# Optimization experiments

Measured on AMD Instinct MI355X. Metric: run time of the kernel, lower is better.

Reference implementation:

```python
import jax, jax.numpy as jnp
import numpy as np
import math

B, N, D = 4, 1024, 1024
H = 16
HD = D // H          # 64
TOP_K = 64
NUM_STATIC = 32


def setup_inputs() -> dict:
    key = jax.random.key(0)
    ks = jax.random.split(key, 10)
    s = 1.0 / math.sqrt(D)  # ~ nn.Linear default init scale
    inp = {
        "x": jax.random.normal(ks[0], (B, N, D), dtype=jnp.float32),
        "Wq": jax.random.uniform(ks[1], (D, D), jnp.float32, -s, s),
        "bq": jax.random.uniform(ks[2], (D,), jnp.float32, -s, s),
        "Wk": jax.random.uniform(ks[3], (D, D), jnp.float32, -s, s),
        "bk": jax.random.uniform(ks[4], (D,), jnp.float32, -s, s),
        "Wv": jax.random.uniform(ks[5], (D, D), jnp.float32, -s, s),
        "bv": jax.random.uniform(ks[6], (D,), jnp.float32, -s, s),
        "Wo": jax.random.uniform(ks[7], (D, D), jnp.float32, -s, s),
        "bo": jax.random.uniform(ks[8], (D,), jnp.float32, -s, s),
        "static_keys": jax.random.normal(ks[9], (NUM_STATIC, D), dtype=jnp.float32),
    }
    return inp


def _heads(t):
    # [B, N, D] -> [B, H, N, HD]
    return t.reshape(B, N, H, HD).transpose(0, 2, 1, 3)


def reference(x, Wq, bq, Wk, bk, Wv, bv, Wo, bo, static_keys):
    Q = _heads(x @ Wq.T + bq)
    K = _heads(x @ Wk.T + bk)
    V = _heads(x @ Wv.T + bv)

    # Replace the first NUM_STATIC key slots with learned static keys.
    K_stat = static_keys.reshape(1, NUM_STATIC, H, HD).transpose(0, 2, 1, 3)  # [1,H,S,HD]
    K_stat = jnp.broadcast_to(K_stat, (B, H, NUM_STATIC, HD))
    K = jnp.concatenate([K_stat, K[:, :, NUM_STATIC:, :]], axis=2)  # [B,H,N,HD]

    scores = jnp.einsum("bhnd,bhmd->bhnm", Q, K) / math.sqrt(HD)  # [B,H,N,N]

    # top-k mask: keep top_k scores per query, -inf elsewhere
    top_scores, top_idx = jax.lax.top_k(scores, TOP_K)  # [B,H,N,K]
    bi = jnp.arange(B)[:, None, None, None]
    hi = jnp.arange(H)[None, :, None, None]
    ni = jnp.arange(N)[None, None, :, None]
    masked = jnp.full(scores.shape, -jnp.inf, dtype=scores.dtype)
    masked = masked.at[bi, hi, ni, top_idx].set(top_scores)

    attn = jax.nn.softmax(masked, axis=-1)
    out = jnp.einsum("bhnm,bhmd->bhnd", attn, V)  # [B,H,N,HD]
    out = out.transpose(0, 2, 1, 3).reshape(B, N, D)
    return out @ Wo.T + bo
```

## Files before the change

### kernel.cpp

```cpp
#include <hip/hip_runtime.h>

#define NSTAT 32
#define MAXSEL 76

typedef __attribute__((ext_vector_type(8))) short bf16x8_t;
typedef __attribute__((ext_vector_type(4))) float f32x4_t;

#define GLOAD_LDS16(g, l) \
    __builtin_amdgcn_global_load_lds((const __attribute__((address_space(1))) void*)(g), \
                                     (__attribute__((address_space(3))) void*)(l), 16, 0, 0)

__device__ __forceinline__ ushort rtn_bf16(float a) {
    unsigned u = __float_as_uint(a);
    return (ushort)((u + 0x7FFFu + ((u >> 16) & 1u)) >> 16);
}
__device__ __forceinline__ void limb2(float a, ushort& h, ushort& l) {
    ushort hh = rtn_bf16(a);
    float fh = __uint_as_float(((unsigned)hh) << 16);
    float r1 = a - fh;
    l = rtn_bf16(r1);
    h = hh;
}

__global__ __launch_bounds__(256)
void decomp_w_kernel(const float* __restrict__ Wq, const float* __restrict__ Wk,
                     const float* __restrict__ Wv, const float* __restrict__ Wo,
                     ushort* __restrict__ WLq, ushort* __restrict__ WoLb)
{
    const int m = blockIdx.y;
    const float* src = (m == 0) ? Wq : (m == 1) ? Wk : (m == 2) ? Wv : Wo;
    const int idx = blockIdx.x * 256 + threadIdx.x;
    const int e8 = idx * 8;
    const int row = e8 >> 10, k0 = e8 & 1023;
    const int kt = k0 >> 5, q = (k0 >> 3) & 3;
    const size_t doff = ((size_t)row << 10) + (size_t)(kt * 32) + (size_t)((q ^ (row & 3)) * 8);

    float4 v0 = *(const float4*)(src + e8);
    float4 v1 = *(const float4*)(src + e8 + 4);
    float f[8] = {v0.x, v0.y, v0.z, v0.w, v1.x, v1.y, v1.z, v1.w};

    const size_t Mi = (size_t)1 << 20;
    ushort h[8], l[8];
    #pragma unroll
    for (int e = 0; e < 8; ++e) limb2(f[e], h[e], l[e]);
    ushort* H = (m == 3) ? WoLb : WLq + (size_t)(m * 2) * Mi;
    ushort* L = H + Mi;
    *(ushort4*)(H + doff)     = make_ushort4(h[0],h[1],h[2],h[3]);
    *(ushort4*)(H + doff + 4) = make_ushort4(h[4],h[5],h[6],h[7]);
    *(ushort4*)(L + doff)     = make_ushort4(l[0],l[1],l[2],l[3]);
    *(ushort4*)(L + doff + 4) = make_ushort4(l[4],l[5],l[6],l[7]);
}

__global__ __launch_bounds__(256, 3)
void limb_gemm_kernel(const float* __restrict__ A,
                      const ushort* __restrict__ WLq, const ushort* __restrict__ WoLb,
                      const float* __restrict__ bq, const float* __restrict__ bk,
                      const float* __restrict__ bv, const float* __restrict__ bo,
                      const float* __restrict__ statk,
                      float* __restrict__ Qw, float* __restrict__ Vw,
                      ushort* __restrict__ KHo, ushort* __restrict__ KLo,
                      float* __restrict__ Cout, int is_out)
{
    __shared__ __align__(16) ushort Al[2][128][32];
    __shared__ __align__(16) ushort Bl[2][2][128][32];

    const int t = threadIdx.x;
    const int bx = blockIdx.x, by = blockIdx.y;
    const int mode = is_out ? 3 : (int)blockIdx.z;
    const int wc0 = bx * 128;
    const int arow0 = by * 128;

    const size_t Mi = (size_t)1 << 20;
    const ushort* BpH;
    const float* bias;
    if (mode == 0)      { BpH = WLq;          bias = bq; }
    else if (mode == 1) { BpH = WLq + 2*Mi;   bias = bk; }
    else if (mode == 2) { BpH = WLq + 4*Mi;   bias = bv; }
    else                { BpH = WoLb;         bias = bo; }
    const ushort* BpL = BpH + Mi;

    const int ll = t & 63, w = t >> 6;

    f32x4_t acc[4][4];
    #pragma unroll
    for (int i = 0; i < 4; ++i)
        #pragma unroll
        for (int j = 0; j < 4; ++j) acc[i][j] = (f32x4_t){0.f, 0.f, 0.f, 0.f};

    auto stageB = [&](int kt, int bb) {
        #pragma unroll
        for (int limb = 0; limb < 2; ++limb) {
            const ushort* src = limb ? BpL : BpH;
            #pragma unroll
            for (int call = 0; call < 2; ++call) {
                int chunk = (w * 2 + call) * 64 + ll;
                int eoff = chunk * 8;
                int row = eoff >> 5, qp = (eoff >> 3) & 3;
                const ushort* g = src + ((size_t)(wc0 + row) << 10) + kt * 32 + qp * 8;
                char* l = ((char*)&Bl[bb][limb][0][0]) + (w * 2 + call) * 1024;
                GLOAD_LDS16(g, l);
            }
        }
    };
    const int srow = t >> 1, skh = (t & 1) * 16;
    auto loadA = [&](int kt, float4* a4) {
        const float* p = A + (((size_t)(arow0 + srow)) << 10) + kt * 32 + skh;
        a4[0] = *(const float4*)(p + 0);
        a4[1] = *(const float4*)(p + 4);
        a4[2] = *(const float4*)(p + 8);
        a4[3] = *(const float4*)(p + 12);
    };
    auto writeA = [&](const float4* a4) {
        float f[16];
        #pragma unroll
        for (int i = 0; i < 4; ++i) {
            f[i*4+0] = a4[i].x; f[i*4+1] = a4[i].y; f[i*4+2] = a4[i].z; f[i*4+3] = a4[i].w;
        }
        ushort h[16], lo[16];
        #pragma unroll
        for (int e = 0; e < 16; ++e) limb2(f[e], h[e], lo[e]);
        const int sw = srow & 3;
        #pragma unroll
        for (int qq = 0; qq < 2; ++qq) {
            int q = (skh >> 3) + qq;
            int qo = (q ^ sw) * 8;
            bf16x8_t vH, vL;
            #pragma unroll
            for (int e = 0; e < 8; ++e) {
                vH[e] = (short)h[qq*8+e]; vL[e] = (short)lo[qq*8+e];
            }
            *(bf16x8_t*)&Al[0][srow][qo] = vH;
            *(bf16x8_t*)&Al[1][srow][qo] = vL;
        }
    };

    const int wr = (w >> 1) * 64, wcv = (w & 1) * 64;
    const int fr = ll & 15, kg = ll >> 4;

    auto compute = [&](int bb) {
        bf16x8_t af[4][2];
        #pragma unroll
        for (int i = 0; i < 4; ++i) {
            int row = wr + i * 16 + fr;
            int qo = (kg ^ (row & 3)) * 8;
            af[i][0] = *(const bf16x8_t*)&Al[0][row][qo];
            af[i][1] = *(const bf16x8_t*)&Al[1][row][qo];
        }
        #pragma unroll
        for (int j = 0; j < 4; ++j) {
            int row = wcv + j * 16 + fr;
            int qo = (kg ^ (row & 3)) * 8;
            bf16x8_t b0 = *(const bf16x8_t*)&Bl[bb][0][row][qo];
            bf16x8_t b1 = *(const bf16x8_t*)&Bl[bb][1][row][qo];
            #pragma unroll
            for (int i = 0; i < 4; ++i) {
                acc[i][j] = __builtin_amdgcn_mfma_f32_16x16x32_bf16(af[i][0], b0, acc[i][j], 0, 0, 0);
                acc[i][j] = __builtin_amdgcn_mfma_f32_16x16x32_bf16(af[i][0], b1, acc[i][j], 0, 0, 0);
                acc[i][j] = __builtin_amdgcn_mfma_f32_16x16x32_bf16(af[i][1], b0, acc[i][j], 0, 0, 0);
            }
        }
    };

    float4 a4[4];
    loadA(0, a4);
    writeA(a4);
    stageB(0, 0);
    __syncthreads();

    float4 a4n[4];
    for (int kt = 0; kt < 32; ++kt) {
        int bb = kt & 1;
        if (kt < 31) {
            stageB(kt + 1, bb ^ 1);
            loadA(kt + 1, a4n);
        }
        compute(bb);
        __syncthreads();
        if (kt < 31) writeA(a4n);
        __syncthreads();
    }

    #pragma unroll
    for (int i = 0; i < 4; ++i) {
        #pragma unroll
        for (int j = 0; j < 4; ++j) {
            int c = wc0 + wcv + j * 16 + (ll & 15);
            float bv_ = bias[c];
            #pragma unroll
            for (int q = 0; q < 4; ++q) {
                int gr = arow0 + wr + i * 16 + (kg) * 4 + q;
                float v = acc[i][j][q] + bv_;
                if (mode == 3) {
                    Cout[(size_t)gr * 1024 + c] = v;
                } else {
                    int b = gr >> 10, n = gr & 1023;
                    int h = c >> 6, d = c & 63;
                    size_t bhn = ((size_t)(b * 16 + h)) * 1024 + n;
                    if (mode == 1) {
                        if (n < NSTAT) v = statk[n * 1024 + c];
                        ushort kh, klo;
                        limb2(v, kh, klo);
                        size_t off = bhn * 64 + (size_t)(((d >> 3) ^ (n & 7)) * 8) + (d & 7);
                        KHo[off] = kh;
                        KLo[off] = klo;
                    } else {
                        float* Out = (mode == 0) ? Qw : Vw;
                        Out[bhn * 64 + d] = v;
                    }
                }
            }
        }
    }
}

__device__ __forceinline__ void radix_stage7(int* __restrict__ hist, int r, int l,
                                             const unsigned* __restrict__ ku,
                                             unsigned pref, unsigned mask, int shift,
                                             int tgt, int2* __restrict__ piv)
{
    #pragma unroll
    for (int b = 0; b < 8; ++b) hist[(l*8 + b)*33 + r] = 0;
    __syncthreads();
    #pragma unroll
    for (int j = 0; j < 64; ++j) {
        unsigned k = ku[j];
        if ((k & mask) == pref)
            atomicAdd(&hist[(int)((k >> shift) & 127u)*33 + r], 1);
    }
    __syncthreads();
    int seg = 0;
    #pragma unroll
    for (int b = 0; b < 8; ++b) seg += hist[(l*8 + b)*33 + r];
    int suf = seg;
    #pragma unroll
    for (int off = 1; off < 16; off <<= 1) {
        int v = __shfl_down(suf, off, 16);
        suf += (l + off < 16) ? v : 0;
    }
    const int above = suf - seg;
    if (above < tgt && above + seg >= tgt) {
        int c = above;
        #pragma unroll
        for (int b = 7; b >= 0; --b) {
            int h = hist[(l*8 + b)*33 + r];
            if (c + h >= tgt) { piv[r] = make_int2(l*8 + b, tgt - c); break; }
            c += h;
        }
    }
    __syncthreads();
}

__global__ __launch_bounds__(512, 4)
void attn_mfma_kernel(const float* __restrict__ Qw,
                      const ushort* __restrict__ KH, const ushort* __restrict__ KL,
                      const float* __restrict__ Vw, float* __restrict__ outp)
{
    __shared__ __align__(16) char pool[59904];
    __shared__ int2 piv[32];
    __shared__ int cnt[32];
    __shared__ float rowsum[32];

    int* hist = (int*)pool;
    float (*Qs)[68] = (float(*)[68])(pool + 32768);
    uint2 (*sel)[MAXSEL] = (uint2(*)[MAXSEL])pool;

    const int t = threadIdx.x;
    const int bid0 = blockIdx.x;
    const int bid = (bid0 & 7) * 256 + (bid0 >> 3);
    const int qt = bid & 31;
    const int bh = bid >> 5;
    const int n0 = qt * 32;
    const float* Qbase = Qw + ((size_t)bh * 1024 + n0) * 64;
    const float* Vbase = Vw + (size_t)bh * 1024 * 64;
    const ushort* KHb = KH + (size_t)bh * 1024 * 64;
    const ushort* KLb = KL + (size_t)bh * 1024 * 64;

    const int ll = t & 63;
    const int w  = t >> 6;
    const int qh = w >> 2;
    const int kr = w & 3;
    const int r  = t >> 4, l = t & 15;

    {
        int q = t >> 4, dq = (t & 15) * 4;
        *(float4*)&Qs[q][dq] = *(const float4*)(Qbase + q * 64 + dq);
    }
    auto stageK = [&](int c, int kb) {
        const ushort* gH = KHb + (size_t)c * 4096 + t * 8;
        const ushort* gL = KLb + (size_t)c * 4096 + t * 8;
        char* dH = pool + kb * 16384 + t * 16;
        char* dL = pool + kb * 16384 + 8192 + t * 16;
        GLOAD_LDS16(gH, dH);
        GLOAD_LDS16(gL, dL);
    };
    stageK(0, 0);
    if (t < 32) cnt[t] = 0;
    __syncthreads();

    bf16x8_t aH[2], aL[2];
    {
        const int arow = qh * 16 + (ll & 15), akg = ll >> 4;
        #pragma unroll
        for (int s = 0; s < 2; ++s) {
            const float* qp = &Qs[arow][s*32 + akg*8];
            float4 q0 = *(const float4*)qp;
            float4 q1 = *(const float4*)(qp + 4);
            float qv[8] = {q0.x,q0.y,q0.z,q0.w,q1.x,q1.y,q1.z,q1.w};
            #pragma unroll
            for (int j = 0; j < 8; ++j) {
                ushort hh, lo2;
                limb2(qv[j], hh, lo2);
                aH[s][j] = (short)hh; aL[s][j] = (short)lo2;
            }
        }
    }

    unsigned ku[64];

    #pragma unroll
    for (int c = 0; c < 16; ++c) {
        const int kb = c & 1;
        float (*scb)[72] = (float(*)[72])(pool + 41472 + kb * 9216);
        if (c < 15) stageK(c + 1, kb ^ 1);

        {
            const ushort* KH_l = (const ushort*)(pool + kb * 16384);
            const ushort* KL_l = KH_l + 4096;
            const int brow = kr * 16 + (ll & 15);
            f32x4_t a_ = {0.f, 0.f, 0.f, 0.f};
            #pragma unroll
            for (int s = 0; s < 2; ++s) {
                int q2 = (s*4 + (ll >> 4)) ^ (brow & 7);
                int off = brow*64 + q2*8;
                bf16x8_t bH = *(const bf16x8_t*)&KH_l[off];
                bf16x8_t bL = *(const bf16x8_t*)&KL_l[off];
                a_ = __builtin_amdgcn_mfma_f32_16x16x32_bf16(aH[s], bH, a_, 0, 0, 0);
                a_ = __builtin_amdgcn_mfma_f32_16x16x32_bf16(aH[s], bL, a_, 0, 0, 0);
                a_ = __builtin_amdgcn_mfma_f32_16x16x32_bf16(aL[s], bH, a_, 0, 0, 0);
            }
            const int qr = qh * 16 + (ll >> 4) * 4;
            scb[qr+0][brow] = a_[0];
            scb[qr+1][brow] = a_[1];
            scb[qr+2][brow] = a_[2];
            scb[qr+3][brow] = a_[3];
        }
        __syncthreads();

        {
            float4 v4 = *(const float4*)&scb[r][l*4];
            float vv[4] = {v4.x, v4.y, v4.z, v4.w};
            #pragma unroll
            for (int e = 0; e < 4; ++e) {
                float vc = fminf(fmaxf(vv[e], -31.9f), 31.9f);
                ku[c*4 + e] = (unsigned)(int)fmaf(vc, 32768.f, 1048576.f);
            }
        }
    }

    int tgt = 64;
    radix_stage7(hist, r, l, ku, 0u, 0u, 14, tgt, piv);
    unsigned pref = (unsigned)piv[r].x << 14; tgt = piv[r].y;
    radix_stage7(hist, r, l, ku, pref, 0x1FC000u, 7, tgt, piv);
    pref |= (unsigned)piv[r].x << 7; tgt = piv[r].y;
    radix_stage7(hist, r, l, ku, pref, 0x1FFF80u, 0, tgt, piv);
    const unsigned thr = pref | (unsigned)piv[r].x;

    const unsigned bhi = thr + 2u;
    const unsigned blo = thr - 2u;
    #pragma unroll
    for (int j = 0; j < 64; ++j) {
        unsigned k = ku[j];
        if (k >= blo) {
            int slot = atomicAdd(&cnt[r], 1);
            if (slot < MAXSEL)
                sel[r][slot] = make_uint2((unsigned)((j >> 2)*64 + l*4 + (j & 3)), k);
        }
    }
    __syncthreads();

    {
        int cc = cnt[r]; cc = (cc < MAXSEL) ? cc : MAXSEL;
        int Dl = 0, ml = 0;
        for (int j = l; j < cc; j += 16) {
            unsigned k = sel[r][j].y;
            if (k > bhi) Dl++; else ml++;
        }
        #pragma unroll
        for (int off = 8; off; off >>= 1) {
            Dl += __shfl_xor(Dl, off, 16);
            ml += __shfl_xor(ml, off, 16);
        }
        const float frac = (float)(64 - Dl) / (float)ml;
        float ls = 0.f;
        for (int j = l; j < cc; j += 16) {
            uint2 p = sel[r][j];
            float wgt = __expf((float)(int)(p.y - thr) * 3.814697265625e-6f);
            if (p.y <= bhi) wgt *= frac;
            p.y = __float_as_uint(wgt);
            sel[r][j] = p;
            ls += wgt;
        }
        #pragma unroll
        for (int off = 8; off; off >>= 1) ls += __shfl_xor(ls, off, 16);
        if (l == 0) { rowsum[r] = ls; cnt[r] = cc; }
    }
    __syncthreads();

    {
        const int pr = t >> 4;
        const int d4 = (t & 15) * 4;
        const int bb = bh >> 4, hh = bh & 15;
        const int cc = cnt[pr];
        float4 a = make_float4(0.f, 0.f, 0.f, 0.f);
        int j = 0;
        for (; j + 1 < cc; j += 2) {
            uint2 p0 = sel[pr][j];
            uint2 p1 = sel[pr][j+1];
            float w0 = __uint_as_float(p0.y);
            float w1 = __uint_as_float(p1.y);
            float4 v0 = *(const float4*)(Vbase + (size_t)p0.x * 64 + d4);
            float4 v1 = *(const float4*)(Vbase + (size_t)p1.x * 64 + d4);
            a.x += w0 * v0.x + w1 * v1.x;
            a.y += w0 * v0.y + w1 * v1.y;
            a.z += w0 * v0.z + w1 * v1.z;
            a.w += w0 * v0.w + w1 * v1.w;
        }
        if (j < cc) {
            uint2 p = sel[pr][j];
            float wv = __uint_as_float(p.y);
            float4 v = *(const float4*)(Vbase + (size_t)p.x * 64 + d4);
            a.x += wv * v.x; a.y += wv * v.y; a.z += wv * v.z; a.w += wv * v.w;
        }
        float inv = 1.0f / rowsum[pr];
        a.x *= inv; a.y *= inv; a.z *= inv; a.w *= inv;
        *(float4*)(outp + ((size_t)bb * 1024 + (n0 + pr)) * 1024 + hh * 64 + d4) = a;
    }
}

extern "C" void kernel_launch(void* const* d_in, const int* in_sizes, int n_in,
                              void* d_out, int out_size, void* d_ws, size_t ws_size,
                              hipStream_t stream) {
    const float* x     = (const float*)d_in[0];
    const float* Wq    = (const float*)d_in[1];
    const float* bq    = (const float*)d_in[2];
    const float* Wk    = (const float*)d_in[3];
    const float* bk    = (const float*)d_in[4];
    const float* Wv    = (const float*)d_in[5];
    const float* bv    = (const float*)d_in[6];
    const float* Wo    = (const float*)d_in[7];
    const float* bo    = (const float*)d_in[8];
    const float* statk = (const float*)d_in[9];
    float* out = (float*)d_out;
    char* base = (char*)d_ws;

    const size_t MiB = (size_t)1 << 20;
    float*  Qw   = (float*)(base);
    float*  Vw   = (float*)(base + 16*MiB);
    ushort* KH   = (ushort*)(base + 32*MiB);
    ushort* KL   = (ushort*)(base + 40*MiB);
    ushort* WoLb = (ushort*)(base + 48*MiB);
    ushort* WLq  = (ushort*)(base + 52*MiB);
    float*  op   = (float*)(base + 52*MiB);

    dim3 gd(512, 4);
    decomp_w_kernel<<<gd, 256, 0, stream>>>(Wq, Wk, Wv, Wo, WLq, WoLb);

    dim3 g1(8, 32, 3);
    limb_gemm_kernel<<<g1, 256, 0, stream>>>(x, WLq, WoLb, bq, bk, bv, bo, statk,
                                             Qw, Vw, KH, KL, nullptr, 0);

    attn_mfma_kernel<<<2048, 512, 0, stream>>>(Qw, KH, KL, Vw, op);

    dim3 g2(8, 32, 1);
    limb_gemm_kernel<<<g2, 256, 0, stream>>>(op, WLq, WoLb, bq, bk, bv, bo, statk,
                                             Qw, Vw, KH, KL, out, 1);
}
```

Before: 320.4 us.

## Keep QK scores in MFMA register layout, process 128-key chunks, drop score LDS buffer

The score loop now handles 128 keys per iteration with two accumulators per wave and packs the MFMA outputs straight into each thread's radix keys. This removes the LDS score transpose buffer and one barrier-mediated round trip per chunk. The radix histograms now index rows by the MFMA layout and keep per-row prefixes for the four rows each thread owns. K staging is single-buffered, with the next chunk loaded after a sync, which shrinks LDS so occupancy can rise (launch bounds 4 to 6 waves) but loses the prefetch overlap with compute.

```diff
diff --git a/kernel.cpp b/kernel.cpp
--- a/kernel.cpp
+++ b/kernel.cpp
@@ -213,53 +213,18 @@
     }
 }
 
-__device__ __forceinline__ void radix_stage7(int* __restrict__ hist, int r, int l,
-                                             const unsigned* __restrict__ ku,
-                                             unsigned pref, unsigned mask, int shift,
-                                             int tgt, int2* __restrict__ piv)
-{
-    #pragma unroll
-    for (int b = 0; b < 8; ++b) hist[(l*8 + b)*33 + r] = 0;
-    __syncthreads();
-    #pragma unroll
-    for (int j = 0; j < 64; ++j) {
-        unsigned k = ku[j];
-        if ((k & mask) == pref)
-            atomicAdd(&hist[(int)((k >> shift) & 127u)*33 + r], 1);
-    }
-    __syncthreads();
-    int seg = 0;
-    #pragma unroll
-    for (int b = 0; b < 8; ++b) seg += hist[(l*8 + b)*33 + r];
-    int suf = seg;
-    #pragma unroll
-    for (int off = 1; off < 16; off <<= 1) {
-        int v = __shfl_down(suf, off, 16);
-        suf += (l + off < 16) ? v : 0;
-    }
-    const int above = suf - seg;
-    if (above < tgt && above + seg >= tgt) {
-        int c = above;
-        #pragma unroll
-        for (int b = 7; b >= 0; --b) {
-            int h = hist[(l*8 + b)*33 + r];
-            if (c + h >= tgt) { piv[r] = make_int2(l*8 + b, tgt - c); break; }
-            c += h;
-        }
-    }
-    __syncthreads();
-}
-
-__global__ __launch_bounds__(512, 4)
+__global__ __launch_bounds__(512, 6)
 void attn_mfma_kernel(const float* __restrict__ Qw,
                       const ushort* __restrict__ KH, const ushort* __restrict__ KL,
                       const float* __restrict__ Vw, float* __restrict__ outp)
 {
-    __shared__ __align__(16) char pool[59904];
+    __shared__ __align__(16) char pool[41472];
     __shared__ int2 piv[32];
     __shared__ int cnt[32];
     __shared__ float rowsum[32];
 
+    ushort* Klds0 = (ushort*)pool;
+    ushort* Klds1 = Klds0 + 8192;
     int* hist = (int*)pool;
     float (*Qs)[68] = (float(*)[68])(pool + 32768);
     uint2 (*sel)[MAXSEL] = (uint2(*)[MAXSEL])pool;
@@ -280,20 +245,22 @@
     const int qh = w >> 2;
     const int kr = w & 3;
     const int r  = t >> 4, l = t & 15;
+    const int qr = qh * 16 + (ll >> 4) * 4;
 
     {
         int q = t >> 4, dq = (t & 15) * 4;
         *(float4*)&Qs[q][dq] = *(const float4*)(Qbase + q * 64 + dq);
     }
-    auto stageK = [&](int c, int kb) {
-        const ushort* gH = KHb + (size_t)c * 4096 + t * 8;
-        const ushort* gL = KLb + (size_t)c * 4096 + t * 8;
-        char* dH = pool + kb * 16384 + t * 16;
-        char* dL = pool + kb * 16384 + 8192 + t * 16;
-        GLOAD_LDS16(gH, dH);
-        GLOAD_LDS16(gL, dL);
-    };
-    stageK(0, 0);
+    auto stageK = [&](int c) {
+        const size_t cb = (size_t)c * 8192;
+        #pragma unroll
+        for (int i = 0; i < 2; ++i) {
+            int boff = i * 8192 + w * 1024;
+            GLOAD_LDS16(KHb + cb + boff / 2 + ll * 8, ((char*)Klds0) + boff);
+            GLOAD_LDS16(KLb + cb + boff / 2 + ll * 8, ((char*)Klds1) + boff);
+        }
+    };
+    stageK(0);
     if (t < 32) cnt[t] = 0;
     __syncthreads();
 
@@ -318,72 +285,107 @@
     unsigned ku[64];
 
     #pragma unroll
-    for (int c = 0; c < 16; ++c) {
-        const int kb = c & 1;
-        float (*scb)[72] = (float(*)[72])(pool + 41472 + kb * 9216);
-        if (c < 15) stageK(c + 1, kb ^ 1);
-
+    for (int c = 0; c < 8; ++c) {
+        f32x4_t acc0 = {0.f,0.f,0.f,0.f}, acc1 = {0.f,0.f,0.f,0.f};
         {
-            const ushort* KH_l = (const ushort*)(pool + kb * 16384);
-            const ushort* KL_l = KH_l + 4096;
-            const int brow = kr * 16 + (ll & 15);
-            f32x4_t a_ = {0.f, 0.f, 0.f, 0.f};
+            const int brow0 = kr * 32 + (ll & 15);
+            const int brow1 = brow0 + 16;
             #pragma unroll
             for (int s = 0; s < 2; ++s) {
-                int q2 = (s*4 + (ll >> 4)) ^ (brow & 7);
-                int off = brow*64 + q2*8;
-                bf16x8_t bH = *(const bf16x8_t*)&KH_l[off];
-                bf16x8_t bL = *(const bf16x8_t*)&KL_l[off];
-                a_ = __builtin_amdgcn_mfma_f32_16x16x32_bf16(aH[s], bH, a_, 0, 0, 0);
-                a_ = __builtin_amdgcn_mfma_f32_16x16x32_bf16(aH[s], bL, a_, 0, 0, 0);
-                a_ = __builtin_amdgcn_mfma_f32_16x16x32_bf16(aL[s], bH, a_, 0, 0, 0);
-            }
-            const int qr = qh * 16 + (ll >> 4) * 4;
-            scb[qr+0][brow] = a_[0];
-            scb[qr+1][brow] = a_[1];
-            scb[qr+2][brow] = a_[2];
-            scb[qr+3][brow] = a_[3];
-        }
-        __syncthreads();
-
-        {
-            float4 v4 = *(const float4*)&scb[r][l*4];
-            float vv[4] = {v4.x, v4.y, v4.z, v4.w};
-            #pragma unroll
-            for (int e = 0; e < 4; ++e) {
-                float vc = fminf(fmaxf(vv[e], -31.9f), 31.9f);
-                ku[c*4 + e] = (unsigned)(int)fmaf(vc, 32768.f, 1048576.f);
-            }
-        }
-    }
-
+                int q20 = (s*4 + (ll >> 4)) ^ (brow0 & 7);
+                int off0 = brow0*64 + q20*8;
+                bf16x8_t bH0 = *(const bf16x8_t*)&Klds0[off0];
+                bf16x8_t bL0 = *(const bf16x8_t*)&Klds1[off0];
+                acc0 = __builtin_amdgcn_mfma_f32_16x16x32_bf16(aH[s], bH0, acc0, 0, 0, 0);
+                acc0 = __builtin_amdgcn_mfma_f32_16x16x32_bf16(aH[s], bL0, acc0, 0, 0, 0);
+                acc0 = __builtin_amdgcn_mfma_f32_16x16x32_bf16(aL[s], bH0, acc0, 0, 0, 0);
+                int q21 = (s*4 + (ll >> 4)) ^ (brow1 & 7);
+                int off1 = brow1*64 + q21*8;
+                bf16x8_t bH1 = *(const bf16x8_t*)&Klds0[off1];
+                bf16x8_t bL1 = *(const bf16x8_t*)&Klds1[off1];
+                acc1 = __builtin_amdgcn_mfma_f32_16x16x32_bf16(aH[s], bH1, acc1, 0, 0, 0);
+                acc1 = __builtin_amdgcn_mfma_f32_16x16x32_bf16(aH[s], bL1, acc1, 0, 0, 0);
+                acc1 = __builtin_amdgcn_mfma_f32_16x16x32_bf16(aL[s], bH1, acc1, 0, 0, 0);
+            }
+        }
+        __syncthreads();
+        if (c < 7) stageK(c + 1);
+        #pragma unroll
+        for (int e = 0; e < 4; ++e) {
+            float v0 = fminf(fmaxf(acc0[e], -31.9f), 31.9f);
+            ku[c*8 + e] = (unsigned)(int)fmaf(v0, 32768.f, 1048576.f);
+            float v1 = fminf(fmaxf(acc1[e], -31.9f), 31.9f);
+            ku[c*8 + 4 + e] = (unsigned)(int)fmaf(v1, 32768.f, 1048576.f);
+        }
+        __syncthreads();
+    }
+
+    unsigned pref4[4] = {0u, 0u, 0u, 0u};
+    unsigned prefc = 0u;
     int tgt = 64;
-    radix_stage7(hist, r, l, ku, 0u, 0u, 14, tgt, piv);
-    unsigned pref = (unsigned)piv[r].x << 14; tgt = piv[r].y;
-    radix_stage7(hist, r, l, ku, pref, 0x1FC000u, 7, tgt, piv);
-    pref |= (unsigned)piv[r].x << 7; tgt = piv[r].y;
-    radix_stage7(hist, r, l, ku, pref, 0x1FFF80u, 0, tgt, piv);
-    const unsigned thr = pref | (unsigned)piv[r].x;
-
-    const unsigned bhi = thr + 2u;
-    const unsigned blo = thr - 2u;
+
+    auto stage = [&](int shift, unsigned mask, bool first) {
+        #pragma unroll
+        for (int b = 0; b < 8; ++b) hist[(l*8 + b)*33 + r] = 0;
+        __syncthreads();
+        #pragma unroll
+        for (int j = 0; j < 64; ++j) {
+            unsigned k = ku[j];
+            if (first || (k & mask) == pref4[j & 3])
+                atomicAdd(&hist[(int)((k >> shift) & 127u)*33 + (qr + (j & 3))], 1);
+        }
+        __syncthreads();
+        int seg = 0;
+        #pragma unroll
+        for (int b = 0; b < 8; ++b) seg += hist[(l*8 + b)*33 + r];
+        int suf = seg;
+        #pragma unroll
+        for (int off = 1; off < 16; off <<= 1) {
+            int v = __shfl_down(suf, off, 16);
+            suf += (l + off < 16) ? v : 0;
+        }
+        const int above = suf - seg;
+        if (above < tgt && above + seg >= tgt) {
+            int cacc = above;
+            #pragma unroll
+            for (int b = 7; b >= 0; --b) {
+                int h = hist[(l*8 + b)*33 + r];
+                if (cacc + h >= tgt) { piv[r] = make_int2(l*8 + b, tgt - cacc); break; }
+                cacc += h;
+            }
+        }
+        __syncthreads();
+        tgt = piv[r].y;
+        prefc |= ((unsigned)piv[r].x) << shift;
+        #pragma unroll
+        for (int e = 0; e < 4; ++e)
+            pref4[e] |= ((unsigned)piv[qr + e].x) << shift;
+    };
+    stage(14, 0u, true);
+    stage(7, 0x1FC000u, false);
+    stage(0, 0x1FFF80u, false);
+
     #pragma unroll
     for (int j = 0; j < 64; ++j) {
         unsigned k = ku[j];
-        if (k >= blo) {
-            int slot = atomicAdd(&cnt[r], 1);
-            if (slot < MAXSEL)
-                sel[r][slot] = make_uint2((unsigned)((j >> 2)*64 + l*4 + (j & 3)), k);
+        if (k >= pref4[j & 3] - 2u) {
+            int row = qr + (j & 3);
+            int slot = atomicAdd(&cnt[row], 1);
+            if (slot < MAXSEL) {
+                unsigned key = (unsigned)((j >> 3)*128 + kr*32 + (((j >> 2) & 1) << 4) + (ll & 15));
+                sel[row][slot] = make_uint2(key, k);
+            }
         }
     }
     __syncthreads();
 
     {
+        const unsigned bhiC = prefc + 2u;
         int cc = cnt[r]; cc = (cc < MAXSEL) ? cc : MAXSEL;
         int Dl = 0, ml = 0;
         for (int j = l; j < cc; j += 16) {
             unsigned k = sel[r][j].y;
-            if (k > bhi) Dl++; else ml++;
+            if (k > bhiC) Dl++; else ml++;
         }
         #pragma unroll
         for (int off = 8; off; off >>= 1) {
@@ -394,8 +396,8 @@
         float ls = 0.f;
         for (int j = l; j < cc; j += 16) {
             uint2 p = sel[r][j];
-            float wgt = __expf((float)(int)(p.y - thr) * 3.814697265625e-6f);
-            if (p.y <= bhi) wgt *= frac;
+            float wgt = __expf((float)(int)(p.y - prefc) * 3.814697265625e-6f);
+            if (p.y <= bhiC) wgt *= frac;
             p.y = __float_as_uint(wgt);
             sel[r][j] = p;
             ls += wgt;
@@ -471,7 +473,7 @@
 
     attn_mfma_kernel<<<2048, 512, 0, stream>>>(Qw, KH, KL, Vw, op);
 
-    dim3 g2(8, 32, 1);
+    dim3 g2(8, 32);
     limb_gemm_kernel<<<g2, 256, 0, stream>>>(op, WLq, WoLb, bq, bk, bv, bo, statk,
                                              Qw, Vw, KH, KL, out, 1);
 }
```

After: 508.1 us. 1.59x slower.

## Process 128-key chunks single-buffered in attention score phase

Applied to the files above, without the earlier changes.

The QK score loop now takes 128-key chunks (8 iterations instead of 16), each wave computing two 16-key MFMA tiles per chunk. It drops double buffering: the next chunk is staged into a single K buffer after the scores are written, overlapping only with the key-conversion step. The aim is to halve the loop iterations and barriers per chunk and to shrink LDS use. In exchange it adds an extra barrier per iteration and leaves less load/compute overlap, so K load latency is more exposed.

```diff
diff --git a/kernel.cpp b/kernel.cpp
--- a/kernel.cpp
+++ b/kernel.cpp
@@ -255,14 +255,17 @@
                       const ushort* __restrict__ KH, const ushort* __restrict__ KL,
                       const float* __restrict__ Vw, float* __restrict__ outp)
 {
-    __shared__ __align__(16) char pool[59904];
+    __shared__ __align__(16) char pool[58368];
     __shared__ int2 piv[32];
     __shared__ int cnt[32];
     __shared__ float rowsum[32];
 
+    ushort* Klds0 = (ushort*)pool;
+    ushort* Klds1 = Klds0 + 8192;
     int* hist = (int*)pool;
-    float (*Qs)[68] = (float(*)[68])(pool + 32768);
-    uint2 (*sel)[MAXSEL] = (uint2(*)[MAXSEL])pool;
+    float (*Qs)[68]  = (float(*)[68])(pool + 32768);
+    float (*sc)[132] = (float(*)[132])(pool + 41472);
+    uint2 (*sel)[MAXSEL] = (uint2(*)[MAXSEL])(pool + 32768);
 
     const int t = threadIdx.x;
     const int bid0 = blockIdx.x;
@@ -285,15 +288,16 @@
         int q = t >> 4, dq = (t & 15) * 4;
         *(float4*)&Qs[q][dq] = *(const float4*)(Qbase + q * 64 + dq);
     }
-    auto stageK = [&](int c, int kb) {
-        const ushort* gH = KHb + (size_t)c * 4096 + t * 8;
-        const ushort* gL = KLb + (size_t)c * 4096 + t * 8;
-        char* dH = pool + kb * 16384 + t * 16;
-        char* dL = pool + kb * 16384 + 8192 + t * 16;
-        GLOAD_LDS16(gH, dH);
-        GLOAD_LDS16(gL, dL);
+    auto stageK = [&](int c) {
+        const size_t cb = (size_t)c * 8192;
+        #pragma unroll
+        for (int i = 0; i < 2; ++i) {
+            int boff = i * 8192 + w * 1024;
+            GLOAD_LDS16(KHb + cb + boff / 2 + ll * 8, ((char*)Klds0) + boff);
+            GLOAD_LDS16(KLb + cb + boff / 2 + ll * 8, ((char*)Klds1) + boff);
+        }
     };
-    stageK(0, 0);
+    stageK(0);
     if (t < 32) cnt[t] = 0;
     __syncthreads();
 
@@ -314,47 +318,48 @@
             }
         }
     }
+    __syncthreads();
 
     unsigned ku[64];
 
     #pragma unroll
-    for (int c = 0; c < 16; ++c) {
-        const int kb = c & 1;
-        float (*scb)[72] = (float(*)[72])(pool + 41472 + kb * 9216);
-        if (c < 15) stageK(c + 1, kb ^ 1);
-
-        {
-            const ushort* KH_l = (const ushort*)(pool + kb * 16384);
-            const ushort* KL_l = KH_l + 4096;
-            const int brow = kr * 16 + (ll & 15);
+    for (int c = 0; c < 8; ++c) {
+        #pragma unroll
+        for (int tile = 0; tile < 2; ++tile) {
+            const int m0 = kr * 32 + tile * 16;
+            const int brow = m0 + (ll & 15);
             f32x4_t a_ = {0.f, 0.f, 0.f, 0.f};
             #pragma unroll
             for (int s = 0; s < 2; ++s) {
                 int q2 = (s*4 + (ll >> 4)) ^ (brow & 7);
                 int off = brow*64 + q2*8;
-                bf16x8_t bH = *(const bf16x8_t*)&KH_l[off];
-                bf16x8_t bL = *(const bf16x8_t*)&KL_l[off];
+                bf16x8_t bH = *(const bf16x8_t*)&Klds0[off];
+                bf16x8_t bL = *(const bf16x8_t*)&Klds1[off];
                 a_ = __builtin_amdgcn_mfma_f32_16x16x32_bf16(aH[s], bH, a_, 0, 0, 0);
                 a_ = __builtin_amdgcn_mfma_f32_16x16x32_bf16(aH[s], bL, a_, 0, 0, 0);
                 a_ = __builtin_amdgcn_mfma_f32_16x16x32_bf16(aL[s], bH, a_, 0, 0, 0);
             }
             const int qr = qh * 16 + (ll >> 4) * 4;
-            scb[qr+0][brow] = a_[0];
-            scb[qr+1][brow] = a_[1];
-            scb[qr+2][brow] = a_[2];
-            scb[qr+3][brow] = a_[3];
+            const int mcol = m0 + (ll & 15);
+            sc[qr+0][mcol] = a_[0];
+            sc[qr+1][mcol] = a_[1];
+            sc[qr+2][mcol] = a_[2];
+            sc[qr+3][mcol] = a_[3];
         }
         __syncthreads();
 
+        if (c < 7) stageK(c + 1);
         {
-            float4 v4 = *(const float4*)&scb[r][l*4];
-            float vv[4] = {v4.x, v4.y, v4.z, v4.w};
-            #pragma unroll
-            for (int e = 0; e < 4; ++e) {
+            float4 v0 = *(const float4*)&sc[r][l*8];
+            float4 v1 = *(const float4*)&sc[r][l*8 + 4];
+            float vv[8] = {v0.x,v0.y,v0.z,v0.w,v1.x,v1.y,v1.z,v1.w};
+            #pragma unroll
+            for (int e = 0; e < 8; ++e) {
                 float vc = fminf(fmaxf(vv[e], -31.9f), 31.9f);
-                ku[c*4 + e] = (unsigned)(int)fmaf(vc, 32768.f, 1048576.f);
-            }
-        }
+                ku[c*8 + e] = (unsigned)(int)fmaf(vc, 32768.f, 1048576.f);
+            }
+        }
+        __syncthreads();
     }
 
     int tgt = 64;
@@ -373,7 +378,7 @@
         if (k >= blo) {
             int slot = atomicAdd(&cnt[r], 1);
             if (slot < MAXSEL)
-                sel[r][slot] = make_uint2((unsigned)((j >> 2)*64 + l*4 + (j & 3)), k);
+                sel[r][slot] = make_uint2((unsigned)((j >> 3)*128 + l*8 + (j & 7)), k);
         }
     }
     __syncthreads();
@@ -471,7 +476,7 @@
 
     attn_mfma_kernel<<<2048, 512, 0, stream>>>(Qw, KH, KL, Vw, op);
 
-    dim3 g2(8, 32, 1);
+    dim3 g2(8, 32);
     limb_gemm_kernel<<<g2, 256, 0, stream>>>(op, WLq, WoLb, bq, bk, bv, bo, statk,
                                              Qw, Vw, KH, KL, out, 1);
 }
```

After: 293.1 us. 1.09x faster.
